# Kernel tuning notes

Measured on AMD Instinct MI355X. Metric: run time of the kernel, lower is better.

## Reference

```python
import jax, jax.numpy as jnp
import numpy as np

B, S, H = 64, 1024, 512
NEG = -1e10


def setup_inputs() -> dict:
    key = jax.random.key(0)
    ks = jax.random.split(key, 10)
    hidden = jax.random.normal(ks[0], (B, H), dtype=jnp.float32)
    encoder_outputs = jax.random.normal(ks[1], (S, B, H), dtype=jnp.float32)
    attn_mask = jax.random.randint(ks[2], (B, S), 0, 2, dtype=jnp.int32)
    src_gps_seqs = jax.random.uniform(ks[3], (S, B, 2), dtype=jnp.float32)
    src = jax.random.uniform(ks[4], (S, B, 3), dtype=jnp.float32)
    src_rids = jax.random.randint(ks[5], (S, B, 1), 0, 10000, dtype=jnp.int64)
    input_id = jax.random.randint(ks[6], (B, 1), 0, 10000, dtype=jnp.int64)
    trg_gps_seqs = jax.random.uniform(ks[7], (B, 2), dtype=jnp.float32)
    # learned params: attn = Linear(2H -> H), v = Linear(H -> 1, no bias)
    bound = 1.0 / np.sqrt(2 * H)
    attn_w = jax.random.uniform(ks[8], (H, 2 * H), minval=-bound, maxval=bound, dtype=jnp.float32)
    attn_b = jnp.zeros((H,), dtype=jnp.float32)
    v_w = jax.random.uniform(ks[9], (1, H), minval=-1.0 / np.sqrt(H), maxval=1.0 / np.sqrt(H), dtype=jnp.float32)
    return {"t": 0, "hidden": hidden, "encoder_outputs": encoder_outputs,
            "attn_mask": attn_mask, "src_gps_seqs": src_gps_seqs, "src": src,
            "src_rids": src_rids, "input_id": input_id, "trg_gps_seqs": trg_gps_seqs,
            "attn_w": attn_w, "attn_b": attn_b, "v_w": v_w}


def reference(t, hidden, encoder_outputs, attn_mask, src_gps_seqs, src,
              src_rids, input_id, trg_gps_seqs, attn_w, attn_b, v_w):
    # encoder_outputs: [S, B, H] -> [B, S, H]
    enc = jnp.transpose(encoder_outputs, (1, 0, 2))
    s_len = enc.shape[1]
    # hidden [B, H] broadcast over src_len -> [B, S, H]
    h = jnp.broadcast_to(hidden[:, None, :], (hidden.shape[0], s_len, hidden.shape[1]))
    cat = jnp.concatenate([h, enc], axis=2)                      # [B, S, 2H]
    energy = jnp.tanh(jnp.einsum('bsk,hk->bsh', cat, attn_w) + attn_b)  # [B, S, H]
    attention = jnp.einsum('bsh,oh->bs', energy, v_w)            # [B, S]
    attention = jnp.where(attn_mask == 0, jnp.float32(NEG), attention)
    return jax.nn.softmax(attention, axis=1)
```

## Files before the change

### kernel.cpp

```cpp
#include <hip/hip_runtime.h>
#include <hip/hip_bf16.h>

typedef unsigned short ushort_t;
typedef unsigned int uint_t;
typedef __attribute__((ext_vector_type(8))) short short8;
typedef __attribute__((ext_vector_type(4))) float f32x4;

#define NEG_VAL -1e10f

#define GL16(gp, lp) __builtin_amdgcn_global_load_lds( \
    (const __attribute__((address_space(1))) uint_t*)(gp), \
    (__attribute__((address_space(3))) uint_t*)(lp), 16, 0, 0)

__device__ __forceinline__ ushort_t f2bf(float x) {
    uint_t u = __float_as_uint(x);
    uint_t r = (u + 0x7fffu + ((u >> 16) & 1u)) >> 16;
    return (ushort_t)r;
}

__device__ __forceinline__ uint_t pkbf(float a, float b) {
    return (uint_t)f2bf(a) | ((uint_t)f2bf(b) << 16);
}

__device__ __forceinline__ uint_t cvtpk(float a, float b) {
    uint_t r;
    asm("v_cvt_pk_bf16_f32 %0, %1, %2" : "=v"(r) : "v"(a), "v"(b));
    return r;
}

__device__ __forceinline__ float tanh_fast(float x) {
    float e = __expf(2.0f * x);
    return 1.0f - 2.0f / (e + 1.0f);
}

__global__ void w2conv_kernel(const float* __restrict__ attn_w, ushort_t* __restrict__ w2) {
    int gid = blockIdx.x * 256 + threadIdx.x;
    int h = gid >> 7, q = gid & 127;
    float4 v = *(const float4*)(attn_w + (size_t)h * 1024 + 512 + q * 4);
    uint2 p;
    p.x = pkbf(v.x, v.y);
    p.y = pkbf(v.z, v.w);
    *(uint2*)(w2 + h * 512 + q * 4) = p;
}

__global__ void hproj_kernel(const float* __restrict__ hidden,
                             const float* __restrict__ attn_w,
                             const float* __restrict__ attn_b,
                             float* __restrict__ hb) {
    int gid = blockIdx.x * 256 + threadIdx.x;
    int b = gid >> 9, h = gid & 511;
    const float4* hp = (const float4*)(hidden + (size_t)b * 512);
    const float4* wp = (const float4*)(attn_w + (size_t)h * 1024);
    float a0 = 0.f, a1 = 0.f, a2 = 0.f, a3 = 0.f;
    #pragma unroll 4
    for (int i = 0; i < 128; i += 4) {
        float4 x0 = hp[i + 0], w0 = wp[i + 0];
        a0 += x0.x * w0.x + x0.y * w0.y + x0.z * w0.z + x0.w * w0.w;
        float4 x1 = hp[i + 1], w1 = wp[i + 1];
        a1 += x1.x * w1.x + x1.y * w1.y + x1.z * w1.z + x1.w * w1.w;
        float4 x2 = hp[i + 2], w2v = wp[i + 2];
        a2 += x2.x * w2v.x + x2.y * w2v.y + x2.z * w2v.z + x2.w * w2v.w;
        float4 x3 = hp[i + 3], w3 = wp[i + 3];
        a3 += x3.x * w3.x + x3.y * w3.y + x3.z * w3.z + x3.w * w3.w;
    }
    hb[gid] = attn_b[h] + ((a0 + a1) + (a2 + a3));
}

__global__ __launch_bounds__(512, 4) void gemm_kernel(
    const float* __restrict__ enc,
    const ushort_t* __restrict__ w2,
    const float* __restrict__ hb,
    const float* __restrict__ vw,
    float* __restrict__ part)
{
    __shared__ __align__(16) float As[2][128 * 32];
    __shared__ __align__(16) ushort_t Bs[2][256 * 32];
    __shared__ float red[4][128];

    const int tid = threadIdx.x;
    const int bid = blockIdx.x;
    const int xcd = bid & 7, j = bid >> 3;
    const int mt = xcd * 64 + (j >> 1), nt = j & 1;
    const size_t m0 = (size_t)mt * 128;
    const int h0 = nt * 256;

    const int wv = tid >> 6, l = tid & 63;
    const int wm = wv >> 2, wn = wv & 3;
    const int lr = l & 15, lq = l >> 4;

    const float* aG = enc + (m0 + (tid >> 3)) * 512 + (((tid & 7) ^ ((tid >> 3) & 7)) << 2);
    const uint_t aLb = (uint_t)__builtin_amdgcn_readfirstlane(wv * 64) * 16;
    const ushort_t* bG = w2 + (size_t)(h0 + (tid >> 2)) * 512 + (((tid & 3) ^ ((tid >> 3) & 3)) << 3);
    const uint_t bLb = aLb;

    const int ra = wm * 64 + lr;
    const uint_t aoff0 = (uint_t)ra * 128 + (uint_t)(((lq * 2 + 0) ^ (ra & 7)) * 16);
    const uint_t aoff1 = (uint_t)ra * 128 + (uint_t)(((lq * 2 + 1) ^ (ra & 7)) * 16);
    const int rb = wn * 64 + lr;
    const uint_t boff = (uint_t)rb * 64 + (uint_t)((lq ^ ((rb >> 1) & 3)) * 16);

    #define STAGE(kt, buf) do { \
        GL16(aG + (kt) * 32,         (char*)(&As[(buf)][0]) + aLb); \
        GL16(aG + (kt) * 32 + 32768, (char*)(&As[(buf)][0]) + aLb + 8192); \
        GL16(bG + (kt) * 32,         (char*)(&Bs[(buf)][0]) + bLb); \
        GL16(bG + (kt) * 32 + 65536, (char*)(&Bs[(buf)][0]) + bLb + 8192); \
    } while (0)

    STAGE(0, 0);
    __syncthreads();

    f32x4 acc[4][4] = {};

    #pragma unroll 2
    for (int kt = 0; kt < 16; ++kt) {
        const int cur = kt & 1;
        if (kt < 15) STAGE(kt + 1, cur ^ 1);
        short8 af[4], bfr[4];
        #pragma unroll
        for (int nf = 0; nf < 4; nf++)
            bfr[nf] = *(const short8*)((const char*)(&Bs[cur][0]) + boff + nf * 1024);
        #pragma unroll
        for (int mf = 0; mf < 4; mf++) {
            f32x4 lo = *(const f32x4*)((const char*)(&As[cur][0]) + aoff0 + mf * 2048);
            f32x4 hi = *(const f32x4*)((const char*)(&As[cur][0]) + aoff1 + mf * 2048);
            union { short8 s; uint_t u[4]; } t;
            t.u[0] = cvtpk(lo[0], lo[1]);
            t.u[1] = cvtpk(lo[2], lo[3]);
            t.u[2] = cvtpk(hi[0], hi[1]);
            t.u[3] = cvtpk(hi[2], hi[3]);
            af[mf] = t.s;
        }
        #pragma unroll
        for (int mf = 0; mf < 4; mf++)
            #pragma unroll
            for (int nf = 0; nf < 4; nf++)
                acc[mf][nf] = __builtin_amdgcn_mfma_f32_16x16x32_bf16(af[mf], bfr[nf], acc[mf][nf], 0, 0, 0);
        __syncthreads();
    }
    #undef STAGE

    float vv[4];
    #pragma unroll
    for (int nf = 0; nf < 4; nf++) vv[nf] = vw[h0 + wn * 64 + nf * 16 + lr];

    #pragma unroll
    for (int mf = 0; mf < 4; mf++) {
        #pragma unroll
        for (int r = 0; r < 4; r++) {
            int row = wm * 64 + mf * 16 + lq * 4 + r;
            int b = row & 63;
            const float* hbp = hb + b * 512 + h0 + wn * 64 + lr;
            float p = 0.f;
            #pragma unroll
            for (int nf = 0; nf < 4; nf++) {
                float x = acc[mf][nf][r] + hbp[nf * 16];
                p += tanh_fast(x) * vv[nf];
            }
            p += __shfl_xor(p, 1);
            p += __shfl_xor(p, 2);
            p += __shfl_xor(p, 4);
            p += __shfl_xor(p, 8);
            if (lr == 0) red[wn][row] = p;
        }
    }
    __syncthreads();
    if (tid < 128) {
        part[(size_t)nt * 65536 + m0 + tid] =
            (red[0][tid] + red[1][tid]) + (red[2][tid] + red[3][tid]);
    }
}

__global__ void softmax_kernel(const float* __restrict__ part,
                               const int* __restrict__ mask,
                               float* __restrict__ out) {
    __shared__ float sred[8];
    int b = blockIdx.x;
    int t = threadIdx.x;
    float vals[4];
    float mx = -INFINITY;
    #pragma unroll
    for (int i = 0; i < 4; i++) {
        int s = t + i * 256;
        int row = s * 64 + b;
        float x = part[row] + part[65536 + row];
        if (mask[b * 1024 + s] == 0) x = NEG_VAL;
        vals[i] = x;
        mx = fmaxf(mx, x);
    }
    #pragma unroll
    for (int o = 32; o; o >>= 1) mx = fmaxf(mx, __shfl_xor(mx, o));
    int w = t >> 6;
    if ((t & 63) == 0) sred[w] = mx;
    __syncthreads();
    mx = fmaxf(fmaxf(sred[0], sred[1]), fmaxf(sred[2], sred[3]));
    float sum = 0.f;
    #pragma unroll
    for (int i = 0; i < 4; i++) {
        vals[i] = __expf(vals[i] - mx);
        sum += vals[i];
    }
    #pragma unroll
    for (int o = 32; o; o >>= 1) sum += __shfl_xor(sum, o);
    if ((t & 63) == 0) sred[4 + w] = sum;
    __syncthreads();
    float tot = (sred[4] + sred[5]) + (sred[6] + sred[7]);
    float inv = 1.0f / tot;
    #pragma unroll
    for (int i = 0; i < 4; i++) out[b * 1024 + t + i * 256] = vals[i] * inv;
}

extern "C" void kernel_launch(void* const* d_in, const int* in_sizes, int n_in,
                              void* d_out, int out_size, void* d_ws, size_t ws_size,
                              hipStream_t stream) {
    const float* hidden = (const float*)d_in[1];
    const float* enc    = (const float*)d_in[2];
    const int*   mask   = (const int*)d_in[3];
    const float* attn_w = (const float*)d_in[9];
    const float* attn_b = (const float*)d_in[10];
    const float* vw     = (const float*)d_in[11];
    float* out = (float*)d_out;

    char* ws = (char*)d_ws;
    ushort_t* w2 = (ushort_t*)ws;
    float* hb   = (float*)(ws + 512 * 1024);
    float* part = (float*)(ws + 640 * 1024);

    w2conv_kernel<<<256, 256, 0, stream>>>(attn_w, w2);
    hproj_kernel<<<128, 256, 0, stream>>>(hidden, attn_w, attn_b, hb);
    gemm_kernel<<<1024, 512, 0, stream>>>(enc, w2, hb, vw, part);
    softmax_kernel<<<64, 256, 0, stream>>>(part, mask, out);
}
```

Measured before the change: 93.45 us.

## Shrink GEMM tile to 128x128 with triple-buffered LDS and explicit vmcnt waits

The fused GEMM+tanh+v-projection kernel goes from 512-thread blocks computing 128x256 tiles to 256-thread blocks computing 128x128 tiles, so the grid doubles. The LDS pipeline moves from double to triple buffering, with manual s_waitcnt vmcnt and raw barriers so two stages of global-to-LDS loads are in flight. MFMA sections are wrapped in s_setprio to favour the matrix work. The aim is better latency hiding and occupancy. The cost is that each fp32 encoder row tile is now fetched by four N-tile blocks instead of two, and the softmax kernel has to sum four partial buffers.

```diff
diff --git a/kernel.cpp b/kernel.cpp
--- a/kernel.cpp
+++ b/kernel.cpp
@@ -66,63 +66,77 @@
     hb[gid] = attn_b[h] + ((a0 + a1) + (a2 + a3));
 }
 
-__global__ __launch_bounds__(512, 4) void gemm_kernel(
+__global__ __launch_bounds__(256, 2) void gemm_kernel(
     const float* __restrict__ enc,
     const ushort_t* __restrict__ w2,
     const float* __restrict__ hb,
     const float* __restrict__ vw,
     float* __restrict__ part)
 {
-    __shared__ __align__(16) float As[2][128 * 32];
-    __shared__ __align__(16) ushort_t Bs[2][256 * 32];
-    __shared__ float red[4][128];
+    __shared__ __align__(16) float As[3][128 * 32];
+    __shared__ __align__(16) ushort_t Bs[3][128 * 32];
+    __shared__ float red[2][128];
 
     const int tid = threadIdx.x;
     const int bid = blockIdx.x;
     const int xcd = bid & 7, j = bid >> 3;
-    const int mt = xcd * 64 + (j >> 1), nt = j & 1;
+    const int mt = xcd * 64 + (j >> 2), nt = j & 3;
     const size_t m0 = (size_t)mt * 128;
-    const int h0 = nt * 256;
+    const int h0 = nt * 128;
 
     const int wv = tid >> 6, l = tid & 63;
-    const int wm = wv >> 2, wn = wv & 3;
+    const int wm = wv >> 1, wn = wv & 1;
     const int lr = l & 15, lq = l >> 4;
 
     const float* aG = enc + (m0 + (tid >> 3)) * 512 + (((tid & 7) ^ ((tid >> 3) & 7)) << 2);
-    const uint_t aLb = (uint_t)__builtin_amdgcn_readfirstlane(wv * 64) * 16;
     const ushort_t* bG = w2 + (size_t)(h0 + (tid >> 2)) * 512 + (((tid & 3) ^ ((tid >> 3) & 3)) << 3);
-    const uint_t bLb = aLb;
-
-    const int ra = wm * 64 + lr;
-    const uint_t aoff0 = (uint_t)ra * 128 + (uint_t)(((lq * 2 + 0) ^ (ra & 7)) * 16);
-    const uint_t aoff1 = (uint_t)ra * 128 + (uint_t)(((lq * 2 + 1) ^ (ra & 7)) * 16);
-    const int rb = wn * 64 + lr;
-    const uint_t boff = (uint_t)rb * 64 + (uint_t)((lq ^ ((rb >> 1) & 3)) * 16);
+    const uint_t sLb = (uint_t)(wv * 64) * 16;
+
+    uint_t aoff0[4], aoff1[4], boff[4];
+    #pragma unroll
+    for (int mf = 0; mf < 4; mf++) {
+        int r = wm * 64 + mf * 16 + lr;
+        aoff0[mf] = (uint_t)r * 128 + (uint_t)(((lq * 2 + 0) ^ (r & 7)) * 16);
+        aoff1[mf] = (uint_t)r * 128 + (uint_t)(((lq * 2 + 1) ^ (r & 7)) * 16);
+    }
+    #pragma unroll
+    for (int nf = 0; nf < 4; nf++) {
+        int r = wn * 64 + nf * 16 + lr;
+        boff[nf] = (uint_t)r * 64 + (uint_t)((lq ^ ((r >> 1) & 3)) * 16);
+    }
 
     #define STAGE(kt, buf) do { \
-        GL16(aG + (kt) * 32,         (char*)(&As[(buf)][0]) + aLb); \
-        GL16(aG + (kt) * 32 + 32768, (char*)(&As[(buf)][0]) + aLb + 8192); \
-        GL16(bG + (kt) * 32,         (char*)(&Bs[(buf)][0]) + bLb); \
-        GL16(bG + (kt) * 32 + 65536, (char*)(&Bs[(buf)][0]) + bLb + 8192); \
+        GL16(aG + (kt) * 32,         (char*)(&As[(buf)][0]) + sLb); \
+        GL16(aG + (kt) * 32 + 16384, (char*)(&As[(buf)][0]) + sLb + 4096); \
+        GL16(aG + (kt) * 32 + 32768, (char*)(&As[(buf)][0]) + sLb + 8192); \
+        GL16(aG + (kt) * 32 + 49152, (char*)(&As[(buf)][0]) + sLb + 12288); \
+        GL16(bG + (kt) * 32,         (char*)(&Bs[(buf)][0]) + sLb); \
+        GL16(bG + (kt) * 32 + 32768, (char*)(&Bs[(buf)][0]) + sLb + 4096); \
     } while (0)
 
     STAGE(0, 0);
-    __syncthreads();
+    STAGE(1, 1);
 
     f32x4 acc[4][4] = {};
 
-    #pragma unroll 2
+    #pragma unroll
     for (int kt = 0; kt < 16; ++kt) {
-        const int cur = kt & 1;
-        if (kt < 15) STAGE(kt + 1, cur ^ 1);
+        const int cur = kt % 3;
+        if (kt < 15) { asm volatile("s_waitcnt vmcnt(6)" ::: "memory"); }
+        else         { asm volatile("s_waitcnt vmcnt(0)" ::: "memory"); }
+        __builtin_amdgcn_s_barrier();
+        __builtin_amdgcn_sched_barrier(0);
+
+        if (kt + 2 <= 15) STAGE(kt + 2, (kt + 2) % 3);
+
         short8 af[4], bfr[4];
         #pragma unroll
         for (int nf = 0; nf < 4; nf++)
-            bfr[nf] = *(const short8*)((const char*)(&Bs[cur][0]) + boff + nf * 1024);
+            bfr[nf] = *(const short8*)((const char*)(&Bs[cur][0]) + boff[nf]);
         #pragma unroll
         for (int mf = 0; mf < 4; mf++) {
-            f32x4 lo = *(const f32x4*)((const char*)(&As[cur][0]) + aoff0 + mf * 2048);
-            f32x4 hi = *(const f32x4*)((const char*)(&As[cur][0]) + aoff1 + mf * 2048);
+            f32x4 lo = *(const f32x4*)((const char*)(&As[cur][0]) + aoff0[mf]);
+            f32x4 hi = *(const f32x4*)((const char*)(&As[cur][0]) + aoff1[mf]);
             union { short8 s; uint_t u[4]; } t;
             t.u[0] = cvtpk(lo[0], lo[1]);
             t.u[1] = cvtpk(lo[2], lo[3]);
@@ -130,12 +144,13 @@
             t.u[3] = cvtpk(hi[2], hi[3]);
             af[mf] = t.s;
         }
+        __builtin_amdgcn_s_setprio(1);
         #pragma unroll
         for (int mf = 0; mf < 4; mf++)
             #pragma unroll
             for (int nf = 0; nf < 4; nf++)
                 acc[mf][nf] = __builtin_amdgcn_mfma_f32_16x16x32_bf16(af[mf], bfr[nf], acc[mf][nf], 0, 0, 0);
-        __syncthreads();
+        __builtin_amdgcn_s_setprio(0);
     }
     #undef STAGE
 
@@ -165,8 +180,7 @@
     }
     __syncthreads();
     if (tid < 128) {
-        part[(size_t)nt * 65536 + m0 + tid] =
-            (red[0][tid] + red[1][tid]) + (red[2][tid] + red[3][tid]);
+        part[(size_t)nt * 65536 + m0 + tid] = red[0][tid] + red[1][tid];
     }
 }
 
@@ -182,7 +196,7 @@
     for (int i = 0; i < 4; i++) {
         int s = t + i * 256;
         int row = s * 64 + b;
-        float x = part[row] + part[65536 + row];
+        float x = part[row] + part[65536 + row] + part[131072 + row] + part[196608 + row];
         if (mask[b * 1024 + s] == 0) x = NEG_VAL;
         vals[i] = x;
         mx = fmaxf(mx, x);
@@ -227,6 +241,6 @@
 
     w2conv_kernel<<<256, 256, 0, stream>>>(attn_w, w2);
     hproj_kernel<<<128, 256, 0, stream>>>(hidden, attn_w, attn_b, hb);
-    gemm_kernel<<<1024, 512, 0, stream>>>(enc, w2, hb, vw, part);
+    gemm_kernel<<<2048, 256, 0, stream>>>(enc, w2, hb, vw, part);
     softmax_kernel<<<64, 256, 0, stream>>>(part, mask, out);
 }
```

Result: slower. 125.8 us (+34.7%).

## Pre-convert encoder outputs to bf16 and use a 256-thread bf16 GEMM

Applied to the files above, without the earlier changes.

Adds a separate pass that converts the fp32 encoder outputs to a bf16 workspace buffer, then runs a new GEMM that stages bf16 A tiles directly and uses 4 waves each computing a 64x128 tile. This removes the in-loop fp32-to-bf16 conversion and halves the A-tile LDS footprint. In exchange it adds a full extra write and read of a 64MB intermediate on a memory-bound workload. The path is used only when the workspace is large enough; otherwise the original fp32 GEMM runs.

```diff
diff --git a/kernel.cpp b/kernel.cpp
--- a/kernel.cpp
+++ b/kernel.cpp
@@ -38,9 +38,21 @@
     int h = gid >> 7, q = gid & 127;
     float4 v = *(const float4*)(attn_w + (size_t)h * 1024 + 512 + q * 4);
     uint2 p;
-    p.x = pkbf(v.x, v.y);
-    p.y = pkbf(v.z, v.w);
+    p.x = cvtpk(v.x, v.y);
+    p.y = cvtpk(v.z, v.w);
     *(uint2*)(w2 + h * 512 + q * 4) = p;
+}
+
+__global__ void aconv_kernel(const float* __restrict__ enc, ushort_t* __restrict__ encb) {
+    size_t base = ((size_t)blockIdx.x * 256 + threadIdx.x) * 8;
+    float4 v0 = *(const float4*)(enc + base);
+    float4 v1 = *(const float4*)(enc + base + 4);
+    uint4 p;
+    p.x = cvtpk(v0.x, v0.y);
+    p.y = cvtpk(v0.z, v0.w);
+    p.z = cvtpk(v1.x, v1.y);
+    p.w = cvtpk(v1.z, v1.w);
+    *(uint4*)(encb + base) = p;
 }
 
 __global__ void hproj_kernel(const float* __restrict__ hidden,
@@ -66,16 +78,16 @@
     hb[gid] = attn_b[h] + ((a0 + a1) + (a2 + a3));
 }
 
-__global__ __launch_bounds__(512, 4) void gemm_kernel(
-    const float* __restrict__ enc,
+__global__ __launch_bounds__(256, 3) void gemma_kernel(
+    const ushort_t* __restrict__ encb,
     const ushort_t* __restrict__ w2,
     const float* __restrict__ hb,
     const float* __restrict__ vw,
     float* __restrict__ part)
 {
-    __shared__ __align__(16) float As[2][128 * 32];
+    __shared__ __align__(16) ushort_t As[2][128 * 32];
     __shared__ __align__(16) ushort_t Bs[2][256 * 32];
-    __shared__ float red[4][128];
+    __shared__ float red[2][128];
 
     const int tid = threadIdx.x;
     const int bid = blockIdx.x;
@@ -85,13 +97,119 @@
     const int h0 = nt * 256;
 
     const int wv = tid >> 6, l = tid & 63;
+    const int wm = wv >> 1, wn = wv & 1;
+    const int lr = l & 15, lq = l >> 4;
+
+    const ushort_t* aG = encb + (m0 + (tid >> 2)) * 512 + (((tid & 3) ^ ((tid >> 3) & 3)) << 3);
+    const ushort_t* bG = w2 + (size_t)(h0 + (tid >> 2)) * 512 + (((tid & 3) ^ ((tid >> 3) & 3)) << 3);
+    const uint_t sLb = (uint_t)(wv * 1024);
+
+    const int raf = wm * 64 + lr;
+    const uint_t aoff0 = (uint_t)raf * 64 + (uint_t)((lq ^ ((raf >> 1) & 3)) * 16);
+    const int rbf = wn * 128 + lr;
+    const uint_t boff0 = (uint_t)rbf * 64 + (uint_t)((lq ^ ((rbf >> 1) & 3)) * 16);
+
+    #define STAGE(kt, buf) do { \
+        GL16(aG + (kt) * 32,         (char*)(&As[(buf)][0]) + sLb); \
+        GL16(aG + (kt) * 32 + 32768, (char*)(&As[(buf)][0]) + sLb + 4096); \
+        GL16(bG + (kt) * 32,         (char*)(&Bs[(buf)][0]) + sLb); \
+        GL16(bG + (kt) * 32 + 32768, (char*)(&Bs[(buf)][0]) + sLb + 4096); \
+        GL16(bG + (kt) * 32 + 65536, (char*)(&Bs[(buf)][0]) + sLb + 8192); \
+        GL16(bG + (kt) * 32 + 98304, (char*)(&Bs[(buf)][0]) + sLb + 12288); \
+    } while (0)
+
+    STAGE(0, 0);
+    __syncthreads();
+
+    f32x4 acc[4][8] = {};
+
+    #pragma unroll 2
+    for (int kt = 0; kt < 16; ++kt) {
+        const int cur = kt & 1;
+        if (kt < 15) STAGE(kt + 1, cur ^ 1);
+        short8 af[4];
+        #pragma unroll
+        for (int mf = 0; mf < 4; mf++)
+            af[mf] = *(const short8*)((const char*)(&As[cur][0]) + aoff0 + mf * 1024);
+        {
+            short8 bfr[4];
+            #pragma unroll
+            for (int nf = 0; nf < 4; nf++)
+                bfr[nf] = *(const short8*)((const char*)(&Bs[cur][0]) + boff0 + nf * 1024);
+            #pragma unroll
+            for (int mf = 0; mf < 4; mf++)
+                #pragma unroll
+                for (int nf = 0; nf < 4; nf++)
+                    acc[mf][nf] = __builtin_amdgcn_mfma_f32_16x16x32_bf16(af[mf], bfr[nf], acc[mf][nf], 0, 0, 0);
+        }
+        {
+            short8 bfr[4];
+            #pragma unroll
+            for (int nf = 0; nf < 4; nf++)
+                bfr[nf] = *(const short8*)((const char*)(&Bs[cur][0]) + boff0 + (nf + 4) * 1024);
+            #pragma unroll
+            for (int mf = 0; mf < 4; mf++)
+                #pragma unroll
+                for (int nf = 0; nf < 4; nf++)
+                    acc[mf][nf + 4] = __builtin_amdgcn_mfma_f32_16x16x32_bf16(af[mf], bfr[nf], acc[mf][nf + 4], 0, 0, 0);
+        }
+        __syncthreads();
+    }
+    #undef STAGE
+
+    float vv[8];
+    #pragma unroll
+    for (int nf = 0; nf < 8; nf++) vv[nf] = vw[h0 + wn * 128 + nf * 16 + lr];
+
+    #pragma unroll
+    for (int mf = 0; mf < 4; mf++) {
+        #pragma unroll
+        for (int r = 0; r < 4; r++) {
+            int row = wm * 64 + mf * 16 + lq * 4 + r;
+            int b = row & 63;
+            const float* hbp = hb + b * 512 + h0 + wn * 128 + lr;
+            float p = 0.f;
+            #pragma unroll
+            for (int nf = 0; nf < 8; nf++) {
+                float x = acc[mf][nf][r] + hbp[nf * 16];
+                p += tanh_fast(x) * vv[nf];
+            }
+            p += __shfl_xor(p, 1);
+            p += __shfl_xor(p, 2);
+            p += __shfl_xor(p, 4);
+            p += __shfl_xor(p, 8);
+            if (lr == 0) red[wn][row] = p;
+        }
+    }
+    __syncthreads();
+    if (tid < 128) {
+        part[(size_t)nt * 65536 + m0 + tid] = red[0][tid] + red[1][tid];
+    }
+}
+
+__global__ __launch_bounds__(512, 4) void gemmf_kernel(
+    const float* __restrict__ enc, const ushort_t* __restrict__ w2,
+    const float* __restrict__ hb, const float* __restrict__ vw,
+    float* __restrict__ part)
+{
+    __shared__ __align__(16) float As[2][128 * 32];
+    __shared__ __align__(16) ushort_t Bs[2][256 * 32];
+    __shared__ float red[4][128];
+
+    const int tid = threadIdx.x;
+    const int bid = blockIdx.x;
+    const int xcd = bid & 7, j = bid >> 3;
+    const int mt = xcd * 64 + (j >> 1), nt = j & 1;
+    const size_t m0 = (size_t)mt * 128;
+    const int h0 = nt * 256;
+
+    const int wv = tid >> 6, l = tid & 63;
     const int wm = wv >> 2, wn = wv & 3;
     const int lr = l & 15, lq = l >> 4;
 
     const float* aG = enc + (m0 + (tid >> 3)) * 512 + (((tid & 7) ^ ((tid >> 3) & 7)) << 2);
     const uint_t aLb = (uint_t)__builtin_amdgcn_readfirstlane(wv * 64) * 16;
     const ushort_t* bG = w2 + (size_t)(h0 + (tid >> 2)) * 512 + (((tid & 3) ^ ((tid >> 3) & 3)) << 3);
-    const uint_t bLb = aLb;
 
     const int ra = wm * 64 + lr;
     const uint_t aoff0 = (uint_t)ra * 128 + (uint_t)(((lq * 2 + 0) ^ (ra & 7)) * 16);
@@ -99,14 +217,14 @@
     const int rb = wn * 64 + lr;
     const uint_t boff = (uint_t)rb * 64 + (uint_t)((lq ^ ((rb >> 1) & 3)) * 16);
 
-    #define STAGE(kt, buf) do { \
+    #define STAGEF(kt, buf) do { \
         GL16(aG + (kt) * 32,         (char*)(&As[(buf)][0]) + aLb); \
         GL16(aG + (kt) * 32 + 32768, (char*)(&As[(buf)][0]) + aLb + 8192); \
-        GL16(bG + (kt) * 32,         (char*)(&Bs[(buf)][0]) + bLb); \
-        GL16(bG + (kt) * 32 + 65536, (char*)(&Bs[(buf)][0]) + bLb + 8192); \
+        GL16(bG + (kt) * 32,         (char*)(&Bs[(buf)][0]) + aLb); \
+        GL16(bG + (kt) * 32 + 65536, (char*)(&Bs[(buf)][0]) + aLb + 8192); \
     } while (0)
 
-    STAGE(0, 0);
+    STAGEF(0, 0);
     __syncthreads();
 
     f32x4 acc[4][4] = {};
@@ -114,7 +232,7 @@
     #pragma unroll 2
     for (int kt = 0; kt < 16; ++kt) {
         const int cur = kt & 1;
-        if (kt < 15) STAGE(kt + 1, cur ^ 1);
+        if (kt < 15) STAGEF(kt + 1, cur ^ 1);
         short8 af[4], bfr[4];
         #pragma unroll
         for (int nf = 0; nf < 4; nf++)
@@ -137,7 +255,7 @@
                 acc[mf][nf] = __builtin_amdgcn_mfma_f32_16x16x32_bf16(af[mf], bfr[nf], acc[mf][nf], 0, 0, 0);
         __syncthreads();
     }
-    #undef STAGE
+    #undef STAGEF
 
     float vv[4];
     #pragma unroll
@@ -222,11 +340,19 @@
 
     char* ws = (char*)d_ws;
     ushort_t* w2 = (ushort_t*)ws;
-    float* hb   = (float*)(ws + 512 * 1024);
-    float* part = (float*)(ws + 640 * 1024);
+    float* hb    = (float*)(ws + 512 * 1024);
+    float* part  = (float*)(ws + 640 * 1024);
+    ushort_t* encb = (ushort_t*)(ws + 1152 * 1024);
+
+    const size_t need = 1152ull * 1024 + 64ull * 1024 * 1024;
 
     w2conv_kernel<<<256, 256, 0, stream>>>(attn_w, w2);
     hproj_kernel<<<128, 256, 0, stream>>>(hidden, attn_w, attn_b, hb);
-    gemm_kernel<<<1024, 512, 0, stream>>>(enc, w2, hb, vw, part);
+    if (ws_size >= need) {
+        aconv_kernel<<<16384, 256, 0, stream>>>(enc, encb);
+        gemma_kernel<<<1024, 256, 0, stream>>>(encb, w2, hb, vw, part);
+    } else {
+        gemmf_kernel<<<1024, 512, 0, stream>>>(enc, w2, hb, vw, part);
+    }
     softmax_kernel<<<64, 256, 0, stream>>>(part, mask, out);
 }
```

Measured after the change: 126.9 us. 1.36x slower.
